# Optimization experiments

Hardware: AMD Instinct MI355X
Metric: run time of the kernel (lower is better)

Reference implementation:

```python
import jax, jax.numpy as jnp
import numpy as np

K = 12
ORDERS = [(1, 2, 3), (1, 3, 2), (3, 2, 1), (3, 1, 2), (2, 1, 3), (2, 3, 1)]


def ranking_3d(x):
    # x: (B, L1, W1, H1, D) -> (B, 12, L1*W1*H1, D)
    B, L1, W1, H1, D = x.shape
    seqs = []
    for dims in ORDERS:
        perm = (0,) + dims + (4,)
        seqs.append(jnp.transpose(x, perm).reshape(B, -1, D))
        xr = jnp.flip(x, axis=dims)
        seqs.append(jnp.transpose(xr, perm).reshape(B, -1, D))
    return jnp.stack(seqs, axis=1)


def restore_original(out_y, shape):
    # out_y: (B, 12, D, L). NOTE: faithfully replicates the original code, which
    # reshapes the (B, D, L) slice directly to (B, d1, d2, d3, D).
    B, L1, W1, H1, D = shape
    size = {1: L1, 2: W1, 3: H1}
    restored = []
    for i in range(12):
        dims = ORDERS[i // 2]
        seq = out_y[:, i]  # (B, D, L)
        dims_shape = tuple(size[d] for d in dims)
        reshaped = seq.reshape((B,) + dims_shape + (D,))
        perm = (0,) + dims + (4,)
        inv = tuple(np.argsort(perm))
        r = jnp.transpose(reshaped, inv)
        if i % 2 == 1:
            r = jnp.flip(r, axis=dims)
        restored.append(r)
    return restored


def selective_scan(u, delta, A, Bs, Cs):
    # u, delta: (B,K,D,L); A: (K,D,N); Bs, Cs: (B,K,N,L)
    us = jnp.moveaxis(u, -1, 0)       # (L,B,K,D)
    ds = jnp.moveaxis(delta, -1, 0)   # (L,B,K,D)
    Bts = jnp.moveaxis(Bs, -1, 0)     # (L,B,K,N)
    Cts = jnp.moveaxis(Cs, -1, 0)     # (L,B,K,N)
    h0 = jnp.zeros(u.shape[:-1] + (A.shape[-1],), u.dtype)  # (B,K,D,N)

    def step(h, inp):
        ut, dt, Bt, Ct = inp
        dA = jnp.exp(dt[..., None] * A)                       # (B,K,D,N)
        h = dA * h + (dt * ut)[..., None] * Bt[:, :, None, :]
        y = jnp.einsum('bkdn,bkn->bkd', h, Ct)
        return h, y

    _, ys = jax.lax.scan(step, h0, (us, ds, Bts, Cts))
    return jnp.moveaxis(ys, 0, -1)  # (B,K,D,L)


def setup_inputs() -> dict:
    key = jax.random.key(0)
    ks = jax.random.split(key, 8)
    B, H, W, Len, D = 1, 16, 16, 16, 128
    N, R = 16, 8
    x = jax.random.normal(ks[0], (B, H, W, Len, D), dtype=jnp.float32)
    x_proj_weight = jax.random.normal(ks[1], (K, R + 2 * N, D), dtype=jnp.float32) * 0.02
    std = R ** -0.5
    dt_projs_weight = jax.random.uniform(ks[2], (K, D, R), minval=-std, maxval=std, dtype=jnp.float32)
    dt = jnp.exp(jax.random.uniform(ks[3], (K, D)) * (np.log(0.1) - np.log(0.001)) + np.log(0.001))
    dt = jnp.clip(dt, 1e-4, None)
    dt_projs_bias = (dt + jnp.log(-jnp.expm1(-dt))).astype(jnp.float32)
    A_logs = jnp.broadcast_to(jnp.log(jnp.arange(1, N + 1, dtype=jnp.float32)), (K, D, N)).copy()
    Ds = jnp.ones((K, D), dtype=jnp.float32)
    merge_w = jax.random.normal(ks[4], (K,), dtype=jnp.float32) * (1.0 / K)
    merge_b = jax.random.normal(ks[5], (), dtype=jnp.float32) * 0.01
    return {'x': x, 'x_proj_weight': x_proj_weight, 'dt_projs_weight': dt_projs_weight,
            'dt_projs_bias': dt_projs_bias, 'A_logs': A_logs, 'Ds': Ds,
            'merge_w': merge_w, 'merge_b': merge_b}


def reference(x, x_proj_weight, dt_projs_weight, dt_projs_bias, A_logs, Ds, merge_w, merge_b):
    B, H, W, Len, D = x.shape
    L = H * W * Len
    R = dt_projs_weight.shape[-1]
    N = A_logs.shape[-1]
    xs = jnp.transpose(ranking_3d(x), (0, 1, 3, 2))  # (B,K,D,L)
    x_dbl = jnp.einsum('bkdl,kcd->bkcl', xs, x_proj_weight)  # (B,K,R+2N,L)
    dts, Bs, Cs = jnp.split(x_dbl, [R, R + N], axis=2)
    dts = jnp.einsum('bkrl,kdr->bkdl', dts, dt_projs_weight)
    delta = jax.nn.softplus(dts + dt_projs_bias[None, :, :, None])
    A = -jnp.exp(A_logs)  # (K,D,N)
    ys = selective_scan(xs, delta, A, Bs, Cs)
    out_y = ys + Ds[None, :, :, None] * xs  # (B,K,D,L)
    restored = restore_original(out_y, (B, H, W, Len, D))
    stacked = jnp.stack(restored, axis=1)  # (B,K,H,W,Len,D)
    # mergeconv: 1x1 Conv2d over K channels == weighted sum across directions
    y = jnp.einsum('bkhwld,k->bhwld', stacked, merge_w) + merge_b
    return y
```

## Files before the change

### kernel.cpp

```cpp
#include <hip/hip_runtime.h>

#define KK 12
#define LL 4096
#define DD 128
#define NN 16
#define RR 8
#define NC 64
#define LC 64
#define XST 132
#define SDST 44
#define XDBL_TILE (64 * SDST)

__device__ __forceinline__ int pos_of(int k, int l) {
    int o = k >> 1;
    int le = (k & 1) ? (4095 - l) : l;
    int t1 = le >> 8, t2 = (le >> 4) & 15, t3 = le & 15;
    switch (o) {
        case 0:  return (t1 << 8) | (t2 << 4) | t3;
        case 1:  return (t1 << 8) | (t3 << 4) | t2;
        case 2:  return (t3 << 8) | (t2 << 4) | t1;
        case 3:  return (t2 << 8) | (t3 << 4) | t1;
        case 4:  return (t2 << 8) | (t1 << 4) | t3;
        default: return (t3 << 8) | (t1 << 4) | t2;
    }
}

__device__ __forceinline__ float delta_row_z(const float* sdbl, int i,
                                             float4 w0, float4 w1, float bz) {
    const float4* dr = (const float4*)(sdbl + i * SDST);
    float4 r0 = dr[0], r1 = dr[1];
    return bz + w0.x * r0.x + w0.y * r0.y + w0.z * r0.z + w0.w * r0.w
              + w1.x * r1.x + w1.y * r1.y + w1.z * r1.z + w1.w * r1.w;
}

__device__ __forceinline__ bool load_A8(const float* __restrict__ A_logs,
                                        int k, int d, int n0, float* A8, float& A0) {
    const float4* ap = (const float4*)(A_logs + ((size_t)(k * DD + d) * NN + n0));
    float4 a0 = ap[0], a1 = ap[1];
    A8[0] = -__expf(a0.x); A8[1] = -__expf(a0.y);
    A8[2] = -__expf(a0.z); A8[3] = -__expf(a0.w);
    A8[4] = -__expf(a1.x); A8[5] = -__expf(a1.y);
    A8[6] = -__expf(a1.z); A8[7] = -__expf(a1.w);
    A0 = -__expf(A_logs[(size_t)(k * DD + d) * NN]);
    bool s = true;
    #pragma unroll
    for (int j = 0; j < 8; j++) {
        float m = (float)(n0 + j + 1);
        s = s && (fabsf(A8[j] - m * A0) <= 1e-4f * m * fabsf(A0));
    }
    return s;
}

template<bool S>
__device__ __forceinline__ void e8_from(float v, float A0, const float* A8,
                                        int half, float* e) {
    if (S) {
        float q = __expf(v * A0);
        float q2 = q * q, q4 = q2 * q2, q8 = q4 * q4;
        e[0] = half ? q8 * q : q;
        #pragma unroll
        for (int j = 1; j < 8; j++) e[j] = e[j - 1] * q;
    } else {
        #pragma unroll
        for (int j = 0; j < 8; j++) e[j] = __expf(v * A8[j]);
    }
}

template<bool S>
__device__ __forceinline__ void scanA_body(
    float* xs, const float* sdbl, int k, int c,
    int d, int half, int n0, const float* A8, float A0,
    float4 w0, float4 w1, float bz, float Dval,
    float* __restrict__ S_g, float* __restrict__ dtsum)
{
    float h[8] = {0, 0, 0, 0, 0, 0, 0, 0};
    float dsum = 0.0f;

    #pragma unroll 4
    for (int i = 0; i < LC; i++) {
        float z = delta_row_z(sdbl, i, w0, w1, bz);
        float E = __expf(-fabsf(z));
        float dt = fmaxf(z, 0.0f) + __logf(1.0f + E);
        float u = xs[i * XST + d];
        dsum += dt;
        float tu = dt * u;
        float e[8];
        e8_from<S>(dt, A0, A8, half, e);
        const float4* bp = (const float4*)(&sdbl[i * SDST + 8 + n0]);
        float4 b0 = bp[0], b1 = bp[1];
        const float4* cp = (const float4*)(&sdbl[i * SDST + 24 + n0]);
        float4 c0 = cp[0], c1 = cp[1];
        h[0] = e[0] * h[0] + tu * b0.x;  h[1] = e[1] * h[1] + tu * b0.y;
        h[2] = e[2] * h[2] + tu * b0.z;  h[3] = e[3] * h[3] + tu * b0.w;
        h[4] = e[4] * h[4] + tu * b1.x;  h[5] = e[5] * h[5] + tu * b1.y;
        h[6] = e[6] * h[6] + tu * b1.z;  h[7] = e[7] * h[7] + tu * b1.w;
        float yp = h[0] * c0.x + h[1] * c0.y + h[2] * c0.z + h[3] * c0.w
                 + h[4] * c1.x + h[5] * c1.y + h[6] * c1.z + h[7] * c1.w;
        float yv = yp + __shfl_xor(yp, 1) + Dval * u;
        if (!half) xs[i * XST + d] = yv;
    }

    float4* sp = (float4*)(S_g + (((size_t)(k * NC + c) * DD + d) * NN + n0));
    sp[0] = make_float4(h[0], h[1], h[2], h[3]);
    sp[1] = make_float4(h[4], h[5], h[6], h[7]);
    if (!half) dtsum[(k * NC + c) * DD + d] = dsum;
}

__global__ __launch_bounds__(256, 3) void k1_proj_scanA(
    const float* __restrict__ x, const float* __restrict__ Wp,
    const float* __restrict__ Wdt, const float* __restrict__ bias,
    const float* __restrict__ A_logs, const float* __restrict__ Ds,
    float* __restrict__ S_g, float* __restrict__ dtsum,
    float* __restrict__ oy, float* __restrict__ xdbl)
{
    const int blk = blockIdx.x;
    const int k = blk >> 6;
    const int c = blk & 63;
    const int l0 = c * LC;
    const int t = threadIdx.x;

    __shared__ __align__(16) float xs[64 * XST];
    __shared__ __align__(16) float sdbl[64 * SDST];
    __shared__ int pos_s[64];

    if (t < 64) pos_s[t] = pos_of(k, l0 + t);
    __syncthreads();

    {
        int lane32 = t & 31, rowi = t >> 5;
        #pragma unroll
        for (int p = 0; p < 8; p++) {
            int l = p * 8 + rowi;
            float4 v = *(const float4*)(x + (size_t)pos_s[l] * DD + lane32 * 4);
            *(float4*)(&xs[l * XST + lane32 * 4]) = v;
        }
    }
    __syncthreads();

    {
        int l = t & 63, cgch = t >> 6;
        float acc[10];
        #pragma unroll
        for (int j = 0; j < 10; j++) acc[j] = 0.0f;
        const float* wk = Wp + (size_t)(k * 40 + cgch * 10) * DD;
        for (int d4 = 0; d4 < DD; d4 += 4) {
            float4 xv = *(const float4*)(&xs[l * XST + d4]);
            #pragma unroll
            for (int j = 0; j < 10; j++) {
                const float* w = wk + j * DD + d4;
                acc[j] += xv.x * w[0] + xv.y * w[1] + xv.z * w[2] + xv.w * w[3];
            }
        }
        #pragma unroll
        for (int j = 0; j < 10; j++) sdbl[l * SDST + cgch * 10 + j] = acc[j];
    }
    __syncthreads();

    if (c != 0) {
        const float4* s4 = (const float4*)sdbl;
        float4* g4 = (float4*)(xdbl + (size_t)blk * XDBL_TILE);
        for (int idx = t; idx < XDBL_TILE / 4; idx += 256) g4[idx] = s4[idx];
    }

    const int d = t >> 1, half = t & 1, n0 = half * 8;
    float A8[8], A0;
    bool structured = load_A8(A_logs, k, d, n0, A8, A0);
    const float4* wp4 = (const float4*)(Wdt + (size_t)(k * DD + d) * RR);
    const float4 w0 = wp4[0], w1 = wp4[1];
    const float bz = bias[k * DD + d];
    const float Dval = Ds[k * DD + d];

    if (structured)
        scanA_body<true>(xs, sdbl, k, c, d, half, n0, A8, A0, w0, w1, bz,
                         Dval, S_g, dtsum);
    else
        scanA_body<false>(xs, sdbl, k, c, d, half, n0, A8, A0, w0, w1, bz,
                          Dval, S_g, dtsum);
    __syncthreads();

    {
        float* base = oy + ((size_t)(k * DD + d)) * LL + l0 + half * 32;
        #pragma unroll
        for (int p = 0; p < 8; p++) {
            int j = p * 4;
            float4 v = make_float4(xs[(half * 32 + j + 0) * XST + d],
                                   xs[(half * 32 + j + 1) * XST + d],
                                   xs[(half * 32 + j + 2) * XST + d],
                                   xs[(half * 32 + j + 3) * XST + d]);
            *(float4*)(base + j) = v;
        }
    }
}

__global__ __launch_bounds__(256) void k2_combine(
    float* __restrict__ S_g, const float* __restrict__ dtsum,
    const float* __restrict__ A_logs)
{
    int tid = blockIdx.x * 256 + threadIdx.x;
    int kk = tid >> 11, rem = tid & 2047, dd2 = rem >> 4;
    float Ac = -__expf(A_logs[tid]);
    float hh = 0.0f;
    #pragma unroll 8
    for (int c2 = 0; c2 < NC; c2++) {
        size_t base = ((size_t)(kk * NC + c2)) * 2048 + rem;
        float s = S_g[base];
        float dsv = dtsum[(kk * NC + c2) * DD + dd2];
        S_g[base] = hh;
        hh = s + __expf(dsv * Ac) * hh;
    }
}

template<bool S>
__device__ __forceinline__ void corr_body(
    float* ybuf, const float* sdbl, int d, int half, int n0,
    const float* A8, float A0, const float* h0, float4 w0, float4 w1, float bz)
{
    float Dsum = 0.0f;
    #pragma unroll 4
    for (int i = 0; i < LC; i++) {
        float z = delta_row_z(sdbl, i, w0, w1, bz);
        float E = __expf(-fabsf(z));
        float dt = fmaxf(z, 0.0f) + __logf(1.0f + E);
        Dsum += dt;
        float e[8];
        e8_from<S>(Dsum, A0, A8, half, e);
        const float4* cp = (const float4*)(&sdbl[i * SDST + 24 + n0]);
        float4 c0 = cp[0], c1 = cp[1];
        float yp = e[0]*h0[0]*c0.x + e[1]*h0[1]*c0.y + e[2]*h0[2]*c0.z + e[3]*h0[3]*c0.w
                 + e[4]*h0[4]*c1.x + e[5]*h0[5]*c1.y + e[6]*h0[6]*c1.z + e[7]*h0[7]*c1.w;
        float yv = yp + __shfl_xor(yp, 1);
        if (!half) ybuf[i * XST + d] = yv;
    }
}

__global__ __launch_bounds__(256, 3) void k3_corr(
    const float* __restrict__ Wdt, const float* __restrict__ bias,
    const float* __restrict__ A_logs, const float* __restrict__ S_g,
    const float* __restrict__ xdbl, float* __restrict__ oy)
{
    const int blk = blockIdx.x;
    const int k = blk >> 6;
    const int c = blk & 63;
    if (c == 0) return;
    const int l0 = c * LC;
    const int t = threadIdx.x;

    __shared__ __align__(16) float sdbl[64 * SDST];
    __shared__ __align__(16) float ybuf[64 * XST];
    {
        const float4* g4 = (const float4*)(xdbl + (size_t)blk * XDBL_TILE);
        float4* s4 = (float4*)sdbl;
        for (int idx = t; idx < XDBL_TILE / 4; idx += 256) s4[idx] = g4[idx];
    }
    __syncthreads();

    const int d = t >> 1, half = t & 1, n0 = half * 8;
    float A8[8], A0;
    bool structured = load_A8(A_logs, k, d, n0, A8, A0);
    const float4* wp4 = (const float4*)(Wdt + (size_t)(k * DD + d) * RR);
    const float4 w0 = wp4[0], w1 = wp4[1];
    const float bz = bias[k * DD + d];

    float h0[8];
    {
        const float4* hp = (const float4*)(S_g + (((size_t)(k * NC + c) * DD + d) * NN + n0));
        float4 h40 = hp[0], h41 = hp[1];
        h0[0] = h40.x; h0[1] = h40.y; h0[2] = h40.z; h0[3] = h40.w;
        h0[4] = h41.x; h0[5] = h41.y; h0[6] = h41.z; h0[7] = h41.w;
    }

    if (structured)
        corr_body<true>(ybuf, sdbl, d, half, n0, A8, A0, h0, w0, w1, bz);
    else
        corr_body<false>(ybuf, sdbl, d, half, n0, A8, A0, h0, w0, w1, bz);
    __syncthreads();

    {
        float* base = oy + ((size_t)(k * DD + d)) * LL + l0 + half * 32;
        #pragma unroll
        for (int p = 0; p < 8; p++) {
            int j = p * 4;
            float4 v = *(float4*)(base + j);
            v.x += ybuf[(half * 32 + j + 0) * XST + d];
            v.y += ybuf[(half * 32 + j + 1) * XST + d];
            v.z += ybuf[(half * 32 + j + 2) * XST + d];
            v.w += ybuf[(half * 32 + j + 3) * XST + d];
            *(float4*)(base + j) = v;
        }
    }
}

__global__ __launch_bounds__(256) void k4_merge(
    const float* __restrict__ out_y, const float* __restrict__ mw,
    const float* __restrict__ mb, float* __restrict__ out)
{
    int idx = blockIdx.x * 256 + threadIdx.x;
    int dd = idx & 127;
    int p = idx >> 7;
    int i3 = p & 15, i2 = (p >> 4) & 15, i1 = (p >> 8) & 15;

    float accv = mb[0];
    #pragma unroll
    for (int k = 0; k < 12; k++) {
        int a1 = i1, a2 = i2, a3 = i3;
        if (k & 1) { a1 = 15 - i1; a2 = 15 - i2; a3 = 15 - i3; }
        int j1, j2, j3;
        switch (k >> 1) {
            case 0:  j1 = a1; j2 = a2; j3 = a3; break;
            case 1:  j1 = a1; j2 = a3; j3 = a2; break;
            case 2:  j1 = a3; j2 = a2; j3 = a1; break;
            case 3:  j1 = a3; j2 = a1; j3 = a2; break;
            case 4:  j1 = a2; j2 = a1; j3 = a3; break;
            default: j1 = a2; j2 = a3; j3 = a1; break;
        }
        int jb = (j1 << 8) | (j2 << 4) | j3;
        accv += mw[k] * out_y[(size_t)k * (DD * LL) + (jb >> 5) * LL
                              + ((jb & 31) << 7) + dd];
    }
    out[idx] = accv;
}

extern "C" void kernel_launch(void* const* d_in, const int* in_sizes, int n_in,
                              void* d_out, int out_size, void* d_ws, size_t ws_size,
                              hipStream_t stream) {
    const float* x      = (const float*)d_in[0];
    const float* Wp     = (const float*)d_in[1];
    const float* Wdt    = (const float*)d_in[2];
    const float* bias   = (const float*)d_in[3];
    const float* A_logs = (const float*)d_in[4];
    const float* Ds     = (const float*)d_in[5];
    const float* mw     = (const float*)d_in[6];
    const float* mb     = (const float*)d_in[7];
    float* out = (float*)d_out;

    float* ws   = (float*)d_ws;
    float* S_g  = ws;
    float* dts  = S_g + (size_t)KK * NC * DD * NN;
    float* oy   = dts + (size_t)KK * NC * DD;
    float* xdbl = oy + (size_t)KK * DD * LL;

    k1_proj_scanA<<<dim3(KK * NC), dim3(256), 0, stream>>>(
        x, Wp, Wdt, bias, A_logs, Ds, S_g, dts, oy, xdbl);
    k2_combine<<<dim3(KK * DD * NN / 256), dim3(256), 0, stream>>>(S_g, dts, A_logs);
    k3_corr<<<dim3(KK * NC), dim3(256), 0, stream>>>(Wdt, bias, A_logs, S_g, xdbl, oy);
    k4_merge<<<dim3(LL * DD / 256), dim3(256), 0, stream>>>(oy, mw, mb, out);
}
```

Baseline: 174.8 us.

## Assign full 16-state scan per thread and split each block into two 32-step chunks

Each thread now keeps all 16 SSM state elements for one channel, so the warp shuffle used to combine two half-state partial sums goes away. The block's 64 positions are split into two independent 32-step sub-chunks, one per half of the threads. This halves the serial scan length but doubles the number of chunks the combine and correction kernels handle. Register pressure per thread roughly doubles, and chunk 0's second half now needs a correction pass.

```diff
diff --git a/kernel.cpp b/kernel.cpp
--- a/kernel.cpp
+++ b/kernel.cpp
@@ -5,8 +5,8 @@
 #define DD 128
 #define NN 16
 #define RR 8
-#define NC 64
-#define LC 64
+#define NC 128
+#define LC 32
 #define XST 132
 #define SDST 44
 #define XDBL_TILE (64 * SDST)
@@ -25,85 +25,92 @@
     }
 }
 
-__device__ __forceinline__ float delta_row_z(const float* sdbl, int i,
+__device__ __forceinline__ float delta_row_z(const float* sdbl, int l,
                                              float4 w0, float4 w1, float bz) {
-    const float4* dr = (const float4*)(sdbl + i * SDST);
+    const float4* dr = (const float4*)(sdbl + l * SDST);
     float4 r0 = dr[0], r1 = dr[1];
     return bz + w0.x * r0.x + w0.y * r0.y + w0.z * r0.z + w0.w * r0.w
               + w1.x * r1.x + w1.y * r1.y + w1.z * r1.z + w1.w * r1.w;
 }
 
-__device__ __forceinline__ bool load_A8(const float* __restrict__ A_logs,
-                                        int k, int d, int n0, float* A8, float& A0) {
-    const float4* ap = (const float4*)(A_logs + ((size_t)(k * DD + d) * NN + n0));
-    float4 a0 = ap[0], a1 = ap[1];
-    A8[0] = -__expf(a0.x); A8[1] = -__expf(a0.y);
-    A8[2] = -__expf(a0.z); A8[3] = -__expf(a0.w);
-    A8[4] = -__expf(a1.x); A8[5] = -__expf(a1.y);
-    A8[6] = -__expf(a1.z); A8[7] = -__expf(a1.w);
-    A0 = -__expf(A_logs[(size_t)(k * DD + d) * NN]);
+__device__ __forceinline__ bool load_A16(const float* __restrict__ A_logs,
+                                         int k, int d, float* A16) {
+    const float4* ap = (const float4*)(A_logs + (size_t)(k * DD + d) * NN);
+    #pragma unroll
+    for (int q = 0; q < 4; q++) {
+        float4 a4 = ap[q];
+        A16[4*q+0] = -__expf(a4.x); A16[4*q+1] = -__expf(a4.y);
+        A16[4*q+2] = -__expf(a4.z); A16[4*q+3] = -__expf(a4.w);
+    }
     bool s = true;
     #pragma unroll
-    for (int j = 0; j < 8; j++) {
-        float m = (float)(n0 + j + 1);
-        s = s && (fabsf(A8[j] - m * A0) <= 1e-4f * m * fabsf(A0));
+    for (int j = 1; j < 16; j++) {
+        float m = (float)(j + 1);
+        s = s && (fabsf(A16[j] - m * A16[0]) <= 1e-4f * m * fabsf(A16[0]));
     }
     return s;
 }
 
 template<bool S>
-__device__ __forceinline__ void e8_from(float v, float A0, const float* A8,
-                                        int half, float* e) {
+__device__ __forceinline__ void e16_from(float v, const float* A16, float* e) {
     if (S) {
-        float q = __expf(v * A0);
-        float q2 = q * q, q4 = q2 * q2, q8 = q4 * q4;
-        e[0] = half ? q8 * q : q;
-        #pragma unroll
-        for (int j = 1; j < 8; j++) e[j] = e[j - 1] * q;
+        float q = __expf(v * A16[0]);
+        e[0] = q;
+        #pragma unroll
+        for (int j = 1; j < 16; j++) e[j] = e[j - 1] * q;
     } else {
         #pragma unroll
-        for (int j = 0; j < 8; j++) e[j] = __expf(v * A8[j]);
+        for (int j = 0; j < 16; j++) e[j] = __expf(v * A16[j]);
     }
 }
 
 template<bool S>
 __device__ __forceinline__ void scanA_body(
-    float* xs, const float* sdbl, int k, int c,
-    int d, int half, int n0, const float* A8, float A0,
-    float4 w0, float4 w1, float bz, float Dval,
+    float* xs, const float* sdbl, int k, int cc, int rbase, int d,
+    const float* A16, float4 w0, float4 w1, float bz, float Dval,
     float* __restrict__ S_g, float* __restrict__ dtsum)
 {
-    float h[8] = {0, 0, 0, 0, 0, 0, 0, 0};
+    float h[16];
+    #pragma unroll
+    for (int n = 0; n < 16; n++) h[n] = 0.0f;
     float dsum = 0.0f;
 
     #pragma unroll 4
     for (int i = 0; i < LC; i++) {
-        float z = delta_row_z(sdbl, i, w0, w1, bz);
+        int l = rbase + i;
+        float z = delta_row_z(sdbl, l, w0, w1, bz);
         float E = __expf(-fabsf(z));
         float dt = fmaxf(z, 0.0f) + __logf(1.0f + E);
-        float u = xs[i * XST + d];
+        float u = xs[l * XST + d];
         dsum += dt;
         float tu = dt * u;
-        float e[8];
-        e8_from<S>(dt, A0, A8, half, e);
-        const float4* bp = (const float4*)(&sdbl[i * SDST + 8 + n0]);
-        float4 b0 = bp[0], b1 = bp[1];
-        const float4* cp = (const float4*)(&sdbl[i * SDST + 24 + n0]);
-        float4 c0 = cp[0], c1 = cp[1];
-        h[0] = e[0] * h[0] + tu * b0.x;  h[1] = e[1] * h[1] + tu * b0.y;
-        h[2] = e[2] * h[2] + tu * b0.z;  h[3] = e[3] * h[3] + tu * b0.w;
-        h[4] = e[4] * h[4] + tu * b1.x;  h[5] = e[5] * h[5] + tu * b1.y;
-        h[6] = e[6] * h[6] + tu * b1.z;  h[7] = e[7] * h[7] + tu * b1.w;
-        float yp = h[0] * c0.x + h[1] * c0.y + h[2] * c0.z + h[3] * c0.w
-                 + h[4] * c1.x + h[5] * c1.y + h[6] * c1.z + h[7] * c1.w;
-        float yv = yp + __shfl_xor(yp, 1) + Dval * u;
-        if (!half) xs[i * XST + d] = yv;
-    }
-
-    float4* sp = (float4*)(S_g + (((size_t)(k * NC + c) * DD + d) * NN + n0));
-    sp[0] = make_float4(h[0], h[1], h[2], h[3]);
-    sp[1] = make_float4(h[4], h[5], h[6], h[7]);
-    if (!half) dtsum[(k * NC + c) * DD + d] = dsum;
+        float e[16];
+        e16_from<S>(dt, A16, e);
+        const float4* bp = (const float4*)(&sdbl[l * SDST + 8]);
+        float4 b0 = bp[0], b1 = bp[1], b2 = bp[2], b3 = bp[3];
+        const float4* cp = (const float4*)(&sdbl[l * SDST + 24]);
+        float4 c0 = cp[0], c1 = cp[1], c2 = cp[2], c3 = cp[3];
+        h[0]  = e[0]  * h[0]  + tu * b0.x;  h[1]  = e[1]  * h[1]  + tu * b0.y;
+        h[2]  = e[2]  * h[2]  + tu * b0.z;  h[3]  = e[3]  * h[3]  + tu * b0.w;
+        h[4]  = e[4]  * h[4]  + tu * b1.x;  h[5]  = e[5]  * h[5]  + tu * b1.y;
+        h[6]  = e[6]  * h[6]  + tu * b1.z;  h[7]  = e[7]  * h[7]  + tu * b1.w;
+        h[8]  = e[8]  * h[8]  + tu * b2.x;  h[9]  = e[9]  * h[9]  + tu * b2.y;
+        h[10] = e[10] * h[10] + tu * b2.z;  h[11] = e[11] * h[11] + tu * b2.w;
+        h[12] = e[12] * h[12] + tu * b3.x;  h[13] = e[13] * h[13] + tu * b3.y;
+        h[14] = e[14] * h[14] + tu * b3.z;  h[15] = e[15] * h[15] + tu * b3.w;
+        float y = h[0]*c0.x + h[1]*c0.y + h[2]*c0.z + h[3]*c0.w
+                + h[4]*c1.x + h[5]*c1.y + h[6]*c1.z + h[7]*c1.w
+                + h[8]*c2.x + h[9]*c2.y + h[10]*c2.z + h[11]*c2.w
+                + h[12]*c3.x + h[13]*c3.y + h[14]*c3.z + h[15]*c3.w;
+        xs[l * XST + d] = y + Dval * u;
+    }
+
+    float4* sp = (float4*)(S_g + (((size_t)(k * NC + cc) * DD + d) * NN));
+    sp[0] = make_float4(h[0],  h[1],  h[2],  h[3]);
+    sp[1] = make_float4(h[4],  h[5],  h[6],  h[7]);
+    sp[2] = make_float4(h[8],  h[9],  h[10], h[11]);
+    sp[3] = make_float4(h[12], h[13], h[14], h[15]);
+    dtsum[(k * NC + cc) * DD + d] = dsum;
 }
 
 __global__ __launch_bounds__(256, 3) void k1_proj_scanA(
@@ -116,7 +123,7 @@
     const int blk = blockIdx.x;
     const int k = blk >> 6;
     const int c = blk & 63;
-    const int l0 = c * LC;
+    const int l0 = c * 64;
     const int t = threadIdx.x;
 
     __shared__ __align__(16) float xs[64 * XST];
@@ -156,37 +163,37 @@
     }
     __syncthreads();
 
-    if (c != 0) {
+    {
         const float4* s4 = (const float4*)sdbl;
         float4* g4 = (float4*)(xdbl + (size_t)blk * XDBL_TILE);
         for (int idx = t; idx < XDBL_TILE / 4; idx += 256) g4[idx] = s4[idx];
     }
 
-    const int d = t >> 1, half = t & 1, n0 = half * 8;
-    float A8[8], A0;
-    bool structured = load_A8(A_logs, k, d, n0, A8, A0);
+    const int d = t & 127, half = t >> 7;
+    const int cc = 2 * c + half, rbase = half * LC;
+    float A16[16];
+    bool structured = load_A16(A_logs, k, d, A16);
     const float4* wp4 = (const float4*)(Wdt + (size_t)(k * DD + d) * RR);
     const float4 w0 = wp4[0], w1 = wp4[1];
     const float bz = bias[k * DD + d];
     const float Dval = Ds[k * DD + d];
 
     if (structured)
-        scanA_body<true>(xs, sdbl, k, c, d, half, n0, A8, A0, w0, w1, bz,
-                         Dval, S_g, dtsum);
+        scanA_body<true>(xs, sdbl, k, cc, rbase, d, A16, w0, w1, bz, Dval,
+                         S_g, dtsum);
     else
-        scanA_body<false>(xs, sdbl, k, c, d, half, n0, A8, A0, w0, w1, bz,
-                          Dval, S_g, dtsum);
-    __syncthreads();
-
-    {
-        float* base = oy + ((size_t)(k * DD + d)) * LL + l0 + half * 32;
+        scanA_body<false>(xs, sdbl, k, cc, rbase, d, A16, w0, w1, bz, Dval,
+                          S_g, dtsum);
+
+    {
+        float* base = oy + ((size_t)(k * DD + d)) * LL + l0 + rbase;
         #pragma unroll
         for (int p = 0; p < 8; p++) {
             int j = p * 4;
-            float4 v = make_float4(xs[(half * 32 + j + 0) * XST + d],
-                                   xs[(half * 32 + j + 1) * XST + d],
-                                   xs[(half * 32 + j + 2) * XST + d],
-                                   xs[(half * 32 + j + 3) * XST + d]);
+            float4 v = make_float4(xs[(rbase + j + 0) * XST + d],
+                                   xs[(rbase + j + 1) * XST + d],
+                                   xs[(rbase + j + 2) * XST + d],
+                                   xs[(rbase + j + 3) * XST + d]);
             *(float4*)(base + j) = v;
         }
     }
@@ -212,24 +219,26 @@
 
 template<bool S>
 __device__ __forceinline__ void corr_body(
-    float* ybuf, const float* sdbl, int d, int half, int n0,
-    const float* A8, float A0, const float* h0, float4 w0, float4 w1, float bz)
+    float* ybuf, const float* sdbl, int rbase, int d,
+    const float* A16, const float* h0, float4 w0, float4 w1, float bz)
 {
     float Dsum = 0.0f;
     #pragma unroll 4
     for (int i = 0; i < LC; i++) {
-        float z = delta_row_z(sdbl, i, w0, w1, bz);
+        int l = rbase + i;
+        float z = delta_row_z(sdbl, l, w0, w1, bz);
         float E = __expf(-fabsf(z));
         float dt = fmaxf(z, 0.0f) + __logf(1.0f + E);
         Dsum += dt;
-        float e[8];
-        e8_from<S>(Dsum, A0, A8, half, e);
-        const float4* cp = (const float4*)(&sdbl[i * SDST + 24 + n0]);
-        float4 c0 = cp[0], c1 = cp[1];
-        float yp = e[0]*h0[0]*c0.x + e[1]*h0[1]*c0.y + e[2]*h0[2]*c0.z + e[3]*h0[3]*c0.w
-                 + e[4]*h0[4]*c1.x + e[5]*h0[5]*c1.y + e[6]*h0[6]*c1.z + e[7]*h0[7]*c1.w;
-        float yv = yp + __shfl_xor(yp, 1);
-        if (!half) ybuf[i * XST + d] = yv;
+        float e[16];
+        e16_from<S>(Dsum, A16, e);
+        const float4* cp = (const float4*)(&sdbl[l * SDST + 24]);
+        float4 c0 = cp[0], c1 = cp[1], c2 = cp[2], c3 = cp[3];
+        float y = e[0]*h0[0]*c0.x + e[1]*h0[1]*c0.y + e[2]*h0[2]*c0.z + e[3]*h0[3]*c0.w
+                + e[4]*h0[4]*c1.x + e[5]*h0[5]*c1.y + e[6]*h0[6]*c1.z + e[7]*h0[7]*c1.w
+                + e[8]*h0[8]*c2.x + e[9]*h0[9]*c2.y + e[10]*h0[10]*c2.z + e[11]*h0[11]*c2.w
+                + e[12]*h0[12]*c3.x + e[13]*h0[13]*c3.y + e[14]*h0[14]*c3.z + e[15]*h0[15]*c3.w;
+        ybuf[l * XST + d] = y;
     }
 }
 
@@ -241,8 +250,7 @@
     const int blk = blockIdx.x;
     const int k = blk >> 6;
     const int c = blk & 63;
-    if (c == 0) return;
-    const int l0 = c * LC;
+    const int l0 = c * 64;
     const int t = threadIdx.x;
 
     __shared__ __align__(16) float sdbl[64 * SDST];
@@ -254,37 +262,42 @@
     }
     __syncthreads();
 
-    const int d = t >> 1, half = t & 1, n0 = half * 8;
-    float A8[8], A0;
-    bool structured = load_A8(A_logs, k, d, n0, A8, A0);
+    const int d = t & 127, half = t >> 7;
+    const int cc = 2 * c + half, rbase = half * LC;
+    float A16[16];
+    bool structured = load_A16(A_logs, k, d, A16);
     const float4* wp4 = (const float4*)(Wdt + (size_t)(k * DD + d) * RR);
     const float4 w0 = wp4[0], w1 = wp4[1];
     const float bz = bias[k * DD + d];
 
-    float h0[8];
-    {
-        const float4* hp = (const float4*)(S_g + (((size_t)(k * NC + c) * DD + d) * NN + n0));
-        float4 h40 = hp[0], h41 = hp[1];
-        h0[0] = h40.x; h0[1] = h40.y; h0[2] = h40.z; h0[3] = h40.w;
-        h0[4] = h41.x; h0[5] = h41.y; h0[6] = h41.z; h0[7] = h41.w;
+    float h0[16];
+    if (cc != 0) {
+        const float4* hp = (const float4*)(S_g + (((size_t)(k * NC + cc) * DD + d) * NN));
+        float4 a = hp[0], b = hp[1], c4 = hp[2], e4 = hp[3];
+        h0[0] = a.x;  h0[1] = a.y;  h0[2] = a.z;  h0[3] = a.w;
+        h0[4] = b.x;  h0[5] = b.y;  h0[6] = b.z;  h0[7] = b.w;
+        h0[8] = c4.x; h0[9] = c4.y; h0[10] = c4.z; h0[11] = c4.w;
+        h0[12] = e4.x; h0[13] = e4.y; h0[14] = e4.z; h0[15] = e4.w;
+    } else {
+        #pragma unroll
+        for (int n = 0; n < 16; n++) h0[n] = 0.0f;
     }
 
     if (structured)
-        corr_body<true>(ybuf, sdbl, d, half, n0, A8, A0, h0, w0, w1, bz);
+        corr_body<true>(ybuf, sdbl, rbase, d, A16, h0, w0, w1, bz);
     else
-        corr_body<false>(ybuf, sdbl, d, half, n0, A8, A0, h0, w0, w1, bz);
-    __syncthreads();
-
-    {
-        float* base = oy + ((size_t)(k * DD + d)) * LL + l0 + half * 32;
+        corr_body<false>(ybuf, sdbl, rbase, d, A16, h0, w0, w1, bz);
+
+    {
+        float* base = oy + ((size_t)(k * DD + d)) * LL + l0 + rbase;
         #pragma unroll
         for (int p = 0; p < 8; p++) {
             int j = p * 4;
             float4 v = *(float4*)(base + j);
-            v.x += ybuf[(half * 32 + j + 0) * XST + d];
-            v.y += ybuf[(half * 32 + j + 1) * XST + d];
-            v.z += ybuf[(half * 32 + j + 2) * XST + d];
-            v.w += ybuf[(half * 32 + j + 3) * XST + d];
+            v.x += ybuf[(rbase + j + 0) * XST + d];
+            v.y += ybuf[(rbase + j + 1) * XST + d];
+            v.z += ybuf[(rbase + j + 2) * XST + d];
+            v.w += ybuf[(rbase + j + 3) * XST + d];
             *(float4*)(base + j) = v;
         }
     }
@@ -339,9 +352,9 @@
     float* oy   = dts + (size_t)KK * NC * DD;
     float* xdbl = oy + (size_t)KK * DD * LL;
 
-    k1_proj_scanA<<<dim3(KK * NC), dim3(256), 0, stream>>>(
+    k1_proj_scanA<<<dim3(KK * 64), dim3(256), 0, stream>>>(
         x, Wp, Wdt, bias, A_logs, Ds, S_g, dts, oy, xdbl);
     k2_combine<<<dim3(KK * DD * NN / 256), dim3(256), 0, stream>>>(S_g, dts, A_logs);
-    k3_corr<<<dim3(KK * NC), dim3(256), 0, stream>>>(Wdt, bias, A_logs, S_g, xdbl, oy);
+    k3_corr<<<dim3(KK * 64), dim3(256), 0, stream>>>(Wdt, bias, A_logs, S_g, xdbl, oy);
     k4_merge<<<dim3(LL * DD / 256), dim3(256), 0, stream>>>(oy, mw, mb, out);
 }
```

Result: faster. 170.4 us (-2.5%).
